# Performance work log

Measured on AMD Instinct MI355X. Metric: run time of the kernel, lower is better.

## Reference

```python
import jax, jax.numpy as jnp
import numpy as np

N, E = 25000, 400000
D_NODE, D_EDGE_IN, D_EH, D_H, D_DUAL = 128, 16, 128, 256, 128


def layer_norm(x, g, b, eps=1e-5):
    mu = jnp.mean(x, axis=-1, keepdims=True)
    var = jnp.mean((x - mu) ** 2, axis=-1, keepdims=True)
    return (x - mu) * jax.lax.rsqrt(var + eps) * g + b


def setup_inputs() -> dict:
    key = jax.random.key(0)
    ks = jax.random.split(key, 20)

    def w(k, shape):
        return (jax.random.normal(k, shape, dtype=jnp.float32) * 0.05)

    inp = {
        "node_embedding": jax.random.normal(ks[0], (N, D_NODE), dtype=jnp.float32),
        "edge_index": jax.random.randint(ks[1], (2, E), 0, N, dtype=jnp.int64),
        "edge_attr": jax.random.normal(ks[2], (E, D_EDGE_IN), dtype=jnp.float32),
        "dual_node_emb": jax.random.normal(ks[3], (E, D_DUAL), dtype=jnp.float32),
        "atom_reactivity_logits": jax.random.normal(ks[4], (N,), dtype=jnp.float32),
        "W_be1": w(ks[5], (D_EDGE_IN, D_EH)), "b_be1": jnp.zeros((D_EH,), jnp.float32),
        "g_be1": jnp.ones((D_EH,), jnp.float32), "bb_be1": jnp.zeros((D_EH,), jnp.float32),
        "W_be2": w(ks[6], (D_EH, D_EH)), "b_be2": jnp.zeros((D_EH,), jnp.float32),
        "g_be2": jnp.ones((D_EH,), jnp.float32), "bb_be2": jnp.zeros((D_EH,), jnp.float32),
        "W_be3": w(ks[7], (D_EH, D_EH)), "b_be3": jnp.zeros((D_EH,), jnp.float32),
        "g_be3": jnp.ones((D_EH,), jnp.float32), "bb_be3": jnp.zeros((D_EH,), jnp.float32),
        # DualGraphBondReactivityPredictor
        "W_d1": w(ks[8], (D_DUAL, D_H)), "b_d1": jnp.zeros((D_H,), jnp.float32),
        "W_d2": w(ks[9], (D_H, D_H)), "b_d2": jnp.zeros((D_H,), jnp.float32),
        "W_do": w(ks[10], (D_H, 1)), "b_do": jnp.zeros((1,), jnp.float32),
        # main head: in = 2*D_NODE + D_EH + 3 = 387
        "W_f1": w(ks[11], (2 * D_NODE + D_EH + 3, D_H)), "b_f1": jnp.zeros((D_H,), jnp.float32),
        "W_f2": w(ks[12], (D_H, D_H)), "b_f2": jnp.zeros((D_H,), jnp.float32),
        "W_bo": w(ks[13], (D_H, 1)), "b_bo": jnp.zeros((1,), jnp.float32),
    }
    return inp


def reference(node_embedding, edge_index, edge_attr, dual_node_emb, atom_reactivity_logits,
              W_be1, b_be1, g_be1, bb_be1, W_be2, b_be2, g_be2, bb_be2,
              W_be3, b_be3, g_be3, bb_be3,
              W_d1, b_d1, W_d2, b_d2, W_do, b_do,
              W_f1, b_f1, W_f2, b_f2, W_bo, b_bo):
    src, dst = edge_index[0], edge_index[1]

    # BondEmbedding (dropout = identity in eval mode)
    e = jax.nn.silu(layer_norm(edge_attr @ W_be1 + b_be1, g_be1, bb_be1))
    e = jax.nn.silu(layer_norm(e @ W_be2 + b_be2, g_be2, bb_be2))
    e = jax.nn.silu(layer_norm(e @ W_be3 + b_be3, g_be3, bb_be3))  # [E, D_EH]

    atom_p = jax.nn.sigmoid(atom_reactivity_logits)  # [N]
    p_src = atom_p[src][:, None]  # [E,1]
    p_dst = atom_p[dst][:, None]

    # dual-graph bond reactivity
    d = jax.nn.silu(dual_node_emb @ W_d1 + b_d1)
    d = jax.nn.silu(d @ W_d2 + b_d2)
    dual_p = jax.nn.sigmoid((d @ W_do + b_do)[:, 0])[:, None]  # [E,1]

    feats = jnp.concatenate(
        [node_embedding[src], node_embedding[dst], e, dual_p, p_src, p_dst], axis=-1
    )  # [E, 2*D_NODE + D_EH + 3]

    x = jax.nn.silu(feats @ W_f1 + b_f1)
    x = jax.nn.silu(x @ W_f2 + b_f2)
    return (x @ W_bo + b_bo)[:, 0]  # [E]
```

## Files before the change

### kernel.cpp

```cpp
#include <hip/hip_runtime.h>
#include <hip/hip_bf16.h>
#include <stdint.h>

typedef __attribute__((ext_vector_type(8))) short bf16x8;
typedef __attribute__((ext_vector_type(4))) float f32x4;
typedef __attribute__((ext_vector_type(4))) float float4v;

__device__ __forceinline__ uint16_t bfc(float x){
    __hip_bfloat16 h = __float2bfloat16(x);
    return __builtin_bit_cast(uint16_t, h);
}
__device__ __forceinline__ uint32_t pk2(float a, float b){
    return (uint32_t)bfc(a) | ((uint32_t)bfc(b) << 16);
}
__device__ __forceinline__ float fsigmoid(float x){ return 1.0f / (1.0f + __expf(-x)); }
__device__ __forceinline__ float fsilu(float x){ return x * fsigmoid(x); }

__device__ __forceinline__ bf16x8 pack8(float4v lo, float4v hi){
    bf16x8 r;
    r[0]=(short)bfc(lo[0]); r[1]=(short)bfc(lo[1]);
    r[2]=(short)bfc(lo[2]); r[3]=(short)bfc(lo[3]);
    r[4]=(short)bfc(hi[0]); r[5]=(short)bfc(hi[1]);
    r[6]=(short)bfc(hi[2]); r[7]=(short)bfc(hi[3]);
    return r;
}

#define SZ_BE1 4096
#define SZ_128 16384
#define SZ_D1  32768
#define SZ_D2  65536
#define SZ_F1  98304
#define OFF_BE1 0
#define OFF_BE2 (OFF_BE1 + SZ_BE1)
#define OFF_BE3 (OFF_BE2 + SZ_128)
#define OFF_D1  (OFF_BE3 + SZ_128)
#define OFF_D2  (OFF_D1 + SZ_D1)
#define OFF_F1  (OFF_D2 + SZ_D2)
#define OFF_F2  (OFF_F1 + SZ_F1)
#define WS_ELEMS (OFF_F2 + SZ_D2)

__device__ __forceinline__ int fragpos(int k, int c, int OUT){
    int kt = k >> 5, ct = c >> 4;
    int fid = kt * (OUT >> 4) + ct;
    int ln = ((k & 31) >> 3) * 16 + (c & 15);
    return fid * 512 + ln * 8 + (k & 7);
}

__global__ void __launch_bounds__(256)
prep_w(const float* __restrict__ Wbe1, const float* __restrict__ Wbe2,
       const float* __restrict__ Wbe3, const float* __restrict__ Wd1,
       const float* __restrict__ Wd2,  const float* __restrict__ Wf1,
       const float* __restrict__ Wf2,  uint16_t* __restrict__ ws){
    int t = blockIdx.x * 256 + threadIdx.x;
    if (t >= WS_ELEMS) return;
    if (t < OFF_BE2) {
        int u = t;            int k = u >> 7, c = u & 127;
        float v = (k < 16) ? Wbe1[k * 128 + c] : 0.0f;
        ws[OFF_BE1 + fragpos(k, c, 128)] = bfc(v);
    } else if (t < OFF_BE3) {
        int u = t - OFF_BE2;  int k = u >> 7, c = u & 127;
        ws[OFF_BE2 + fragpos(k, c, 128)] = bfc(Wbe2[u]);
    } else if (t < OFF_D1) {
        int u = t - OFF_BE3;  int k = u >> 7, c = u & 127;
        ws[OFF_BE3 + fragpos(k, c, 128)] = bfc(Wbe3[u]);
    } else if (t < OFF_D2) {
        int u = t - OFF_D1;   int k = u >> 8, c = u & 255;
        ws[OFF_D1 + fragpos(k, c, 256)] = bfc(Wd1[u]);
    } else if (t < OFF_F1) {
        int u = t - OFF_D2;   int k = u >> 8, c = u & 255;
        ws[OFF_D2 + fragpos(k, c, 256)] = bfc(Wd2[u]);
    } else if (t < OFF_F2) {
        int u = t - OFF_F1;   int k = u >> 8, c = u & 255;
        ws[OFF_F1 + fragpos(k, c, 256)] = bfc(Wf1[u]);
    } else {
        int u = t - OFF_F2;   int k = u >> 8, c = u & 255;
        ws[OFF_F2 + fragpos(k, c, 256)] = bfc(Wf2[u]);
    }
}

__global__ void __launch_bounds__(256)
prep_n(const float* __restrict__ src, uint16_t* __restrict__ dst, int n){
    int t = blockIdx.x * 256 + threadIdx.x;
    if (t < n) dst[t] = bfc(src[t]);
}

typedef const __attribute__((address_space(1))) void gas_void;
typedef __attribute__((address_space(3))) void las_void;
__device__ __forceinline__ void g2l16(const void* g, void* l){
    __builtin_amdgcn_global_load_lds((gas_void*)g, (las_void*)l, 16, 0, 0);
}

#define LDS_TOTAL 135168

__global__ void __launch_bounds__(512) __attribute__((amdgpu_waves_per_eu(2, 2)))
bond_fast_kernel(const int* __restrict__ edge_index,
                 const float* __restrict__ edge_attr, const float* __restrict__ dual_emb,
                 const float* __restrict__ logits,
                 const float* __restrict__ b_be1, const float* __restrict__ g_be1, const float* __restrict__ bb_be1,
                 const float* __restrict__ b_be2, const float* __restrict__ g_be2, const float* __restrict__ bb_be2,
                 const float* __restrict__ b_be3, const float* __restrict__ g_be3, const float* __restrict__ bb_be3,
                 const float* __restrict__ b_d1, const float* __restrict__ b_d2,
                 const float* __restrict__ W_do, const float* __restrict__ b_do,
                 const float* __restrict__ W_f1, const float* __restrict__ b_f1,
                 const float* __restrict__ b_f2,
                 const float* __restrict__ W_bo, const float* __restrict__ b_bo,
                 const uint16_t* __restrict__ ws, float* __restrict__ out, int E)
{
    __shared__ char lds[LDS_TOTAL];
    const int t    = threadIdx.x;
    const int wave = t >> 6;
    const int lane = t & 63;
    const int li   = lane & 15, lg = lane >> 4;
    const int eg   = wave >> 1;
    const int ch   = wave & 1;
    const int e0b  = blockIdx.x * 128;

    char* bufE = lds;
    char* h256 = lds + 32768;
    uint16_t* wb0 = (uint16_t*)(lds + 98304);
    uint16_t* wb1 = (uint16_t*)(lds + 114688);
    float* ps  = (float*)(lds + 131072);
    float* pd  = (float*)(lds + 131584);
    int* sidx  = (int*)(lds + 132096);
    int* didx  = (int*)(lds + 132608);
    float* dpp = (float*)(lds + 133120);
    float* bop = (float*)(lds + 134144);

    const uint8_t*  wsb = (const uint8_t*)ws;
    const uint16_t* nbf = ws + WS_ELEMS;

    if (t < 128) {
        int e = e0b + t; if (e >= E) e = E - 1;
        int s_ = edge_index[e];
        int d_ = edge_index[E + e];
        sidx[t] = s_; didx[t] = d_;
        ps[t] = fsigmoid(logits[s_]);
        pd[t] = fsigmoid(logits[d_]);
    }

    int cur = 0;
    auto stageW = [&](int elemoff, int big){
        uint8_t* dst = (uint8_t*)(cur ? wb0 : wb1) + t * 16;
        const uint8_t* g = wsb + (size_t)elemoff * 2 + t * 16;
        g2l16(g, dst);
        if (big) g2l16(g + 8192, dst + 8192);
    };
    auto stepend = [&](){ __syncthreads(); cur ^= 1; };
    auto curbuf  = [&]() -> const uint16_t* { return cur ? wb1 : wb0; };

    f32x4 acc[2][8];

    auto ldf = [&](const uint16_t* w, int fid) -> bf16x8 {
        return *(const bf16x8*)(w + fid * 512 + lane * 8);
    };
    auto grpBE = [&](const uint16_t* w, bf16x8 a0){
        #pragma unroll
        for (int ct = 0; ct < 8; ++ct){
            bf16x8 b = ldf(w, ct);
            acc[0][ct] = __builtin_amdgcn_mfma_f32_16x16x32_bf16(a0, b, acc[0][ct], 0, 0, 0);
        }
    };
    auto grp256 = [&](const uint16_t* w, bf16x8 a0, bf16x8 a1){
        #pragma unroll
        for (int ct = 0; ct < 8; ++ct){
            bf16x8 b = ldf(w, ch * 8 + ct);
            acc[0][ct] = __builtin_amdgcn_mfma_f32_16x16x32_bf16(a0, b, acc[0][ct], 0, 0, 0);
            acc[1][ct] = __builtin_amdgcn_mfma_f32_16x16x32_bf16(a1, b, acc[1][ct], 0, 0, 0);
        }
    };
    auto initBE = [&](const float* b){
        #pragma unroll
        for (int ct = 0; ct < 8; ++ct){
            float bv = b[li + 16 * ct];
            f32x4 iv = {bv, bv, bv, bv};
            acc[0][ct] = iv;
        }
    };
    auto init256 = [&](const float* b){
        #pragma unroll
        for (int ct = 0; ct < 8; ++ct){
            float bv = b[ch * 128 + ct * 16 + li];
            f32x4 iv = {bv, bv, bv, bv};
            acc[0][ct] = iv; acc[1][ct] = iv;
        }
    };
    auto eb_read = [&](int row, int kt) -> bf16x8 {
        int off = row * 256 + (kt * 32 + lg * 8) * 2;
        return *(const bf16x8*)(bufE + (off ^ ((row & 7) << 4)));
    };
    auto h2_read = [&](int row, int kt) -> bf16x8 {
        int off = row * 512 + (kt * 32 + lg * 8) * 2;
        return *(const bf16x8*)(h256 + (off ^ ((row & 7) << 4)));
    };
    auto lnstoreBE = [&](const float* g, const float* bb){
        #pragma unroll
        for (int r = 0; r < 4; ++r){
            float s = 0.f, q = 0.f;
            #pragma unroll
            for (int ct = 0; ct < 8; ++ct){ float v = acc[0][ct][r]; s += v; q += v*v; }
            s += __shfl_xor(s, 1); q += __shfl_xor(q, 1);
            s += __shfl_xor(s, 2); q += __shfl_xor(q, 2);
            s += __shfl_xor(s, 4); q += __shfl_xor(q, 4);
            s += __shfl_xor(s, 8); q += __shfl_xor(q, 8);
            float mu = s * 0.0078125f;
            float var = q * 0.0078125f - mu * mu;
            float rs = rsqrtf(var + 1e-5f);
            int row = wave * 16 + lg * 4 + r;
            int rswz = (row & 7) << 4;
            #pragma unroll
            for (int ct = 0; ct < 8; ++ct){
                int col = li + 16 * ct;
                float v = (acc[0][ct][r] - mu) * rs * g[col] + bb[col];
                int off = row * 256 + col * 2;
                *(uint16_t*)(bufE + (off ^ rswz)) = bfc(fsilu(v));
            }
        }
    };
    auto silustore256 = [&](){
        #pragma unroll
        for (int rt = 0; rt < 2; ++rt){
            #pragma unroll
            for (int r = 0; r < 4; ++r){
                int row = eg * 32 + rt * 16 + lg * 4 + r;
                int rswz = (row & 7) << 4;
                #pragma unroll
                for (int ct = 0; ct < 8; ++ct){
                    int off = row * 512 + (ch * 128 + ct * 16 + li) * 2;
                    *(uint16_t*)(h256 + (off ^ rswz)) = bfc(fsilu(acc[rt][ct][r]));
                }
            }
        }
    };

    {
        const uint8_t* g = wsb + t * 16;
        g2l16(g, (uint8_t*)wb0 + t * 16);
    }
    __syncthreads();

    {
        stageW(OFF_BE2, 0);
        bf16x8 aE = {0,0,0,0,0,0,0,0};
        if (lg < 2){
            int ea = e0b + wave * 16 + li; if (ea >= E) ea = E - 1;
            const float* pa = edge_attr + (size_t)ea * 16 + lg * 8;
            aE = pack8(*(const float4v*)pa, *(const float4v*)(pa + 4));
        }
        initBE(b_be1);
        grpBE(curbuf(), aE);
        lnstoreBE(g_be1, bb_be1);
        stepend();
    }

    initBE(b_be2);
    #pragma unroll
    for (int kt = 0; kt < 4; ++kt){
        if (kt < 3) stageW(OFF_BE2 + (kt + 1) * 4096, 0);
        else        stageW(OFF_BE3, 0);
        grpBE(curbuf(), eb_read(wave * 16 + li, kt));
        if (kt == 3) lnstoreBE(g_be2, bb_be2);
        stepend();
    }
    initBE(b_be3);
    #pragma unroll
    for (int kt = 0; kt < 4; ++kt){
        if (kt < 3) stageW(OFF_BE3 + (kt + 1) * 4096, 0);
        else        stageW(OFF_D1, 1);
        grpBE(curbuf(), eb_read(wave * 16 + li, kt));
        if (kt == 3) lnstoreBE(g_be3, bb_be3);
        stepend();
    }

    init256(b_d1);
    #pragma unroll
    for (int kt = 0; kt < 4; ++kt){
        float4v va0, va1, vb0, vb1;
        {
            int ea = e0b + eg * 32 + li;      if (ea >= E) ea = E - 1;
            int eb = e0b + eg * 32 + 16 + li; if (eb >= E) eb = E - 1;
            const float* pa = dual_emb + (size_t)ea * 128 + kt * 32 + lg * 8;
            const float* pb = dual_emb + (size_t)eb * 128 + kt * 32 + lg * 8;
            va0 = *(const float4v*)pa; va1 = *(const float4v*)(pa + 4);
            vb0 = *(const float4v*)pb; vb1 = *(const float4v*)(pb + 4);
        }
        if (kt < 3) stageW(OFF_D1 + (kt + 1) * 8192, 1);
        else        stageW(OFF_D2, 1);
        grp256(curbuf(), pack8(va0, va1), pack8(vb0, vb1));
        if (kt == 3) silustore256();
        stepend();
    }

    init256(b_d2);
    #pragma unroll
    for (int kt = 0; kt < 8; ++kt){
        if (kt < 7) stageW(OFF_D2 + (kt + 1) * 8192, 1);
        else        stageW(OFF_F1, 1);
        grp256(curbuf(), h2_read(eg * 32 + li, kt), h2_read(eg * 32 + 16 + li, kt));
        if (kt == 7){
            #pragma unroll
            for (int rt = 0; rt < 2; ++rt){
                #pragma unroll
                for (int r = 0; r < 4; ++r){
                    float s = 0.f;
                    #pragma unroll
                    for (int ct = 0; ct < 8; ++ct)
                        s += fsilu(acc[rt][ct][r]) * W_do[ch * 128 + ct * 16 + li];
                    s += __shfl_xor(s, 1); s += __shfl_xor(s, 2);
                    s += __shfl_xor(s, 4); s += __shfl_xor(s, 8);
                    if (li == 0) dpp[ch * 128 + eg * 32 + rt * 16 + lg * 4 + r] = s;
                }
            }
        }
        stepend();
    }

    {
        {
            float bdo0 = b_do[0];
            #pragma unroll
            for (int ct = 0; ct < 8; ++ct){
                int col = ch * 128 + ct * 16 + li;
                float bv = b_f1[col];
                float t0 = W_f1[384 * 256 + col];
                float t1 = W_f1[385 * 256 + col];
                float t2 = W_f1[386 * 256 + col];
                #pragma unroll
                for (int rt = 0; rt < 2; ++rt)
                    #pragma unroll
                    for (int r = 0; r < 4; ++r){
                        int row = eg * 32 + rt * 16 + lg * 4 + r;
                        float dv = fsigmoid(dpp[row] + dpp[128 + row] + bdo0);
                        acc[rt][ct][r] = bv + dv*t0 + ps[row]*t1 + pd[row]*t2;
                    }
            }
        }
        int s0 = sidx[eg * 32 + li],      s1 = sidx[eg * 32 + 16 + li];
        int d0 = didx[eg * 32 + li],      d1 = didx[eg * 32 + 16 + li];
        #pragma unroll
        for (int kt = 0; kt < 12; ++kt){
            bf16x8 a0, a1;
            if (kt < 8){
                int ra = (kt < 4) ? s0 : d0;
                int rb = (kt < 4) ? s1 : d1;
                int ko = (kt & 3) * 32 + lg * 8;
                a0 = *(const bf16x8*)(nbf + (size_t)ra * 128 + ko);
                a1 = *(const bf16x8*)(nbf + (size_t)rb * 128 + ko);
            } else {
                a0 = eb_read(eg * 32 + li, kt - 8);
                a1 = eb_read(eg * 32 + 16 + li, kt - 8);
            }
            if (kt < 11) stageW(OFF_F1 + (kt + 1) * 8192, 1);
            else         stageW(OFF_F2, 1);
            grp256(curbuf(), a0, a1);
            if (kt == 11) silustore256();
            stepend();
        }
    }

    init256(b_f2);
    #pragma unroll
    for (int kt = 0; kt < 8; ++kt){
        if (kt < 7) stageW(OFF_F2 + (kt + 1) * 8192, 1);
        grp256(curbuf(), h2_read(eg * 32 + li, kt), h2_read(eg * 32 + 16 + li, kt));
        if (kt == 7){
            #pragma unroll
            for (int rt = 0; rt < 2; ++rt){
                #pragma unroll
                for (int r = 0; r < 4; ++r){
                    float s = 0.f;
                    #pragma unroll
                    for (int ct = 0; ct < 8; ++ct)
                        s += fsilu(acc[rt][ct][r]) * W_bo[ch * 128 + ct * 16 + li];
                    s += __shfl_xor(s, 1); s += __shfl_xor(s, 2);
                    s += __shfl_xor(s, 4); s += __shfl_xor(s, 8);
                    if (li == 0) bop[ch * 128 + eg * 32 + rt * 16 + lg * 4 + r] = s;
                }
            }
        } else {
            stepend();
        }
    }
    __syncthreads();
    if (t < 128){
        int e = e0b + t;
        if (e < E) out[e] = bop[t] + bop[128 + t] + b_bo[0];
    }
}

__global__ void __launch_bounds__(512) __attribute__((amdgpu_waves_per_eu(2, 2)))
bond_fused_kernel(const float* __restrict__ node_emb, const int* __restrict__ edge_index,
                  const float* __restrict__ edge_attr, const float* __restrict__ dual_emb,
                  const float* __restrict__ logits,
                  const float* __restrict__ W_be1, const float* __restrict__ b_be1,
                  const float* __restrict__ g_be1, const float* __restrict__ bb_be1,
                  const float* __restrict__ W_be2, const float* __restrict__ b_be2,
                  const float* __restrict__ g_be2, const float* __restrict__ bb_be2,
                  const float* __restrict__ W_be3, const float* __restrict__ b_be3,
                  const float* __restrict__ g_be3, const float* __restrict__ bb_be3,
                  const float* __restrict__ W_d1, const float* __restrict__ b_d1,
                  const float* __restrict__ W_d2, const float* __restrict__ b_d2,
                  const float* __restrict__ W_do, const float* __restrict__ b_do,
                  const float* __restrict__ W_f1, const float* __restrict__ b_f1,
                  const float* __restrict__ W_f2, const float* __restrict__ b_f2,
                  const float* __restrict__ W_bo, const float* __restrict__ b_bo,
                  float* __restrict__ out, int E)
{
    __shared__ char lds[LDS_TOTAL];
    const int t    = threadIdx.x;
    const int wave = t >> 6;
    const int lane = t & 63;
    const int li   = lane & 15, lg = lane >> 4;
    const int eg   = wave >> 1;
    const int ch   = wave & 1;
    const int e0b  = blockIdx.x * 128;

    char* bufE = lds;
    char* h256 = lds + 32768;
    uint16_t* wb0 = (uint16_t*)(lds + 98304);
    uint16_t* wb1 = (uint16_t*)(lds + 114688);
    float* ps  = (float*)(lds + 131072);
    float* pd  = (float*)(lds + 131584);
    int* sidx  = (int*)(lds + 132096);
    int* didx  = (int*)(lds + 132608);
    float* dpp = (float*)(lds + 133120);
    float* bop = (float*)(lds + 134144);

    if (t < 128) {
        int e = e0b + t; if (e >= E) e = E - 1;
        int s_ = edge_index[e];
        int d_ = edge_index[E + e];
        sidx[t] = s_; didx[t] = d_;
        ps[t] = fsigmoid(logits[s_]);
        pd[t] = fsigmoid(logits[d_]);
    }

    float sr[2][8];
    auto issueW256 = [&](const float* W, int kbase){
        #pragma unroll
        for (int h = 0; h < 2; ++h){
            const float* p = W + (size_t)(kbase + lg * 8) * 256 + (wave + 8*h) * 16 + li;
            #pragma unroll
            for (int j = 0; j < 8; ++j) sr[h][j] = p[j * 256];
        }
    };
    auto issueW128 = [&](const float* W, int kbase, int K){
        const float* p = W + (size_t)(kbase + lg * 8) * 128 + wave * 16 + li;
        #pragma unroll
        for (int j = 0; j < 8; ++j)
            sr[0][j] = (kbase + lg * 8 + j < K) ? p[j * 128] : 0.f;
    };
    auto commitW = [&](uint16_t* dst, int nh){
        #pragma unroll
        for (int h = 0; h < 2; ++h){
            if (h < nh){
                uint4 w;
                w.x = pk2(sr[h][0], sr[h][1]); w.y = pk2(sr[h][2], sr[h][3]);
                w.z = pk2(sr[h][4], sr[h][5]); w.w = pk2(sr[h][6], sr[h][7]);
                *(uint4*)(dst + (wave + 8*h) * 512 + lane * 8) = w;
            }
        }
    };

    int cur = 0;
    auto stepend = [&](int mode){
        if (mode) commitW(cur ? wb0 : wb1, mode == 128 ? 1 : 2);
        __syncthreads();
        cur ^= 1;
    };
    auto curbuf = [&]() -> const uint16_t* { return cur ? wb1 : wb0; };

    f32x4 acc[2][8];

    auto ldf = [&](const uint16_t* w, int fid) -> bf16x8 {
        return *(const bf16x8*)(w + fid * 512 + lane * 8);
    };
    auto grpBE = [&](const uint16_t* w, bf16x8 a0){
        #pragma unroll
        for (int ct = 0; ct < 8; ++ct){
            bf16x8 b = ldf(w, ct);
            acc[0][ct] = __builtin_amdgcn_mfma_f32_16x16x32_bf16(a0, b, acc[0][ct], 0, 0, 0);
        }
    };
    auto grp256 = [&](const uint16_t* w, bf16x8 a0, bf16x8 a1){
        #pragma unroll
        for (int ct = 0; ct < 8; ++ct){
            bf16x8 b = ldf(w, ch * 8 + ct);
            acc[0][ct] = __builtin_amdgcn_mfma_f32_16x16x32_bf16(a0, b, acc[0][ct], 0, 0, 0);
            acc[1][ct] = __builtin_amdgcn_mfma_f32_16x16x32_bf16(a1, b, acc[1][ct], 0, 0, 0);
        }
    };
    auto initBE = [&](const float* b){
        #pragma unroll
        for (int ct = 0; ct < 8; ++ct){
            float bv = b[li + 16 * ct];
            f32x4 iv = {bv, bv, bv, bv};
            acc[0][ct] = iv;
        }
    };
    auto init256 = [&](const float* b){
        #pragma unroll
        for (int ct = 0; ct < 8; ++ct){
            float bv = b[ch * 128 + ct * 16 + li];
            f32x4 iv = {bv, bv, bv, bv};
            acc[0][ct] = iv; acc[1][ct] = iv;
        }
    };
    auto eb_read = [&](int row, int kt) -> bf16x8 {
        int off = row * 256 + (kt * 32 + lg * 8) * 2;
        return *(const bf16x8*)(bufE + (off ^ ((row & 7) << 4)));
    };
    auto h2_read = [&](int row, int kt) -> bf16x8 {
        int off = row * 512 + (kt * 32 + lg * 8) * 2;
        return *(const bf16x8*)(h256 + (off ^ ((row & 7) << 4)));
    };
    auto lnstoreBE = [&](const float* g, const float* bb){
        #pragma unroll
        for (int r = 0; r < 4; ++r){
            float s = 0.f, q = 0.f;
            #pragma unroll
            for (int ct = 0; ct < 8; ++ct){ float v = acc[0][ct][r]; s += v; q += v*v; }
            s += __shfl_xor(s, 1); q += __shfl_xor(q, 1);
            s += __shfl_xor(s, 2); q += __shfl_xor(q, 2);
            s += __shfl_xor(s, 4); q += __shfl_xor(q, 4);
            s += __shfl_xor(s, 8); q += __shfl_xor(q, 8);
            float mu = s * 0.0078125f;
            float var = q * 0.0078125f - mu * mu;
            float rs = rsqrtf(var + 1e-5f);
            int row = wave * 16 + lg * 4 + r;
            int rswz = (row & 7) << 4;
            #pragma unroll
            for (int ct = 0; ct < 8; ++ct){
                int col = li + 16 * ct;
                float v = (acc[0][ct][r] - mu) * rs * g[col] + bb[col];
                int off = row * 256 + col * 2;
                *(uint16_t*)(bufE + (off ^ rswz)) = bfc(fsilu(v));
            }
        }
    };
    auto silustore256 = [&](){
        #pragma unroll
        for (int rt = 0; rt < 2; ++rt){
            #pragma unroll
            for (int r = 0; r < 4; ++r){
                int row = eg * 32 + rt * 16 + lg * 4 + r;
                int rswz = (row & 7) << 4;
                #pragma unroll
                for (int ct = 0; ct < 8; ++ct){
                    int off = row * 512 + (ch * 128 + ct * 16 + li) * 2;
                    *(uint16_t*)(h256 + (off ^ rswz)) = bfc(fsilu(acc[rt][ct][r]));
                }
            }
        }
    };

    issueW128(W_be1, 0, 16);
    commitW(wb0, 1);
    __syncthreads();

    {
        bf16x8 aE = {0,0,0,0,0,0,0,0};
        if (lg < 2){
            int ea = e0b + wave * 16 + li; if (ea >= E) ea = E - 1;
            const float* pa = edge_attr + (size_t)ea * 16 + lg * 8;
            aE = pack8(*(const float4v*)pa, *(const float4v*)(pa + 4));
        }
        issueW128(W_be2, 0, 128);
        initBE(b_be1);
        grpBE(curbuf(), aE);
        lnstoreBE(g_be1, bb_be1);
        stepend(128);
    }

    initBE(b_be2);
    #pragma unroll 1
    for (int kt = 0; kt < 4; ++kt){
        if (kt < 3) issueW128(W_be2, (kt + 1) * 32, 128);
        else        issueW128(W_be3, 0, 128);
        grpBE(curbuf(), eb_read(wave * 16 + li, kt));
        if (kt == 3) lnstoreBE(g_be2, bb_be2);
        stepend(128);
    }
    initBE(b_be3);
    #pragma unroll 1
    for (int kt = 0; kt < 4; ++kt){
        if (kt < 3) issueW128(W_be3, (kt + 1) * 32, 128);
        else        issueW256(W_d1, 0);
        grpBE(curbuf(), eb_read(wave * 16 + li, kt));
        if (kt == 3) lnstoreBE(g_be3, bb_be3);
        stepend(kt < 3 ? 128 : 256);
    }

    init256(b_d1);
    #pragma unroll 1
    for (int kt = 0; kt < 4; ++kt){
        float4v va0, va1, vb0, vb1;
        {
            int ea = e0b + eg * 32 + li;      if (ea >= E) ea = E - 1;
            int eb = e0b + eg * 32 + 16 + li; if (eb >= E) eb = E - 1;
            const float* pa = dual_emb + (size_t)ea * 128 + kt * 32 + lg * 8;
            const float* pb = dual_emb + (size_t)eb * 128 + kt * 32 + lg * 8;
            va0 = *(const float4v*)pa; va1 = *(const float4v*)(pa + 4);
            vb0 = *(const float4v*)pb; vb1 = *(const float4v*)(pb + 4);
        }
        if (kt < 3) issueW256(W_d1, (kt + 1) * 32);
        else        issueW256(W_d2, 0);
        grp256(curbuf(), pack8(va0, va1), pack8(vb0, vb1));
        if (kt == 3) silustore256();
        stepend(256);
    }

    init256(b_d2);
    #pragma unroll 1
    for (int kt = 0; kt < 8; ++kt){
        if (kt < 7) issueW256(W_d2, (kt + 1) * 32);
        else        issueW256(W_f1, 0);
        grp256(curbuf(), h2_read(eg * 32 + li, kt), h2_read(eg * 32 + 16 + li, kt));
        if (kt == 7){
            #pragma unroll
            for (int rt = 0; rt < 2; ++rt){
                #pragma unroll
                for (int r = 0; r < 4; ++r){
                    float s = 0.f;
                    #pragma unroll
                    for (int ct = 0; ct < 8; ++ct)
                        s += fsilu(acc[rt][ct][r]) * W_do[ch * 128 + ct * 16 + li];
                    s += __shfl_xor(s, 1); s += __shfl_xor(s, 2);
                    s += __shfl_xor(s, 4); s += __shfl_xor(s, 8);
                    if (li == 0) dpp[ch * 128 + eg * 32 + rt * 16 + lg * 4 + r] = s;
                }
            }
        }
        stepend(256);
    }

    {
        {
            float bdo0 = b_do[0];
            #pragma unroll
            for (int ct = 0; ct < 8; ++ct){
                int col = ch * 128 + ct * 16 + li;
                float bv = b_f1[col];
                float t0 = W_f1[384 * 256 + col];
                float t1 = W_f1[385 * 256 + col];
                float t2 = W_f1[386 * 256 + col];
                #pragma unroll
                for (int rt = 0; rt < 2; ++rt)
                    #pragma unroll
                    for (int r = 0; r < 4; ++r){
                        int row = eg * 32 + rt * 16 + lg * 4 + r;
                        float dv = fsigmoid(dpp[row] + dpp[128 + row] + bdo0);
                        acc[rt][ct][r] = bv + dv*t0 + ps[row]*t1 + pd[row]*t2;
                    }
            }
        }
        int s0 = sidx[eg * 32 + li],      s1 = sidx[eg * 32 + 16 + li];
        int d0 = didx[eg * 32 + li],      d1 = didx[eg * 32 + 16 + li];
        #pragma unroll 1
        for (int kt = 0; kt < 12; ++kt){
            bf16x8 a0, a1;
            if (kt < 8){
                int ra = (kt < 4) ? s0 : d0;
                int rb = (kt < 4) ? s1 : d1;
                int ko = (kt & 3) * 32 + lg * 8;
                const float* pa = node_emb + (size_t)ra * 128 + ko;
                const float* pb = node_emb + (size_t)rb * 128 + ko;
                a0 = pack8(*(const float4v*)pa, *(const float4v*)(pa + 4));
                a1 = pack8(*(const float4v*)pb, *(const float4v*)(pb + 4));
            } else {
                a0 = eb_read(eg * 32 + li, kt - 8);
                a1 = eb_read(eg * 32 + 16 + li, kt - 8);
            }
            if (kt < 11) issueW256(W_f1, (kt + 1) * 32);
            else         issueW256(W_f2, 0);
            grp256(curbuf(), a0, a1);
            if (kt == 11) silustore256();
            stepend(256);
        }
    }

    init256(b_f2);
    #pragma unroll 1
    for (int kt = 0; kt < 8; ++kt){
        if (kt < 7) issueW256(W_f2, (kt + 1) * 32);
        grp256(curbuf(), h2_read(eg * 32 + li, kt), h2_read(eg * 32 + 16 + li, kt));
        if (kt == 7){
            #pragma unroll
            for (int rt = 0; rt < 2; ++rt){
                #pragma unroll
                for (int r = 0; r < 4; ++r){
                    float s = 0.f;
                    #pragma unroll
                    for (int ct = 0; ct < 8; ++ct)
                        s += fsilu(acc[rt][ct][r]) * W_bo[ch * 128 + ct * 16 + li];
                    s += __shfl_xor(s, 1); s += __shfl_xor(s, 2);
                    s += __shfl_xor(s, 4); s += __shfl_xor(s, 8);
                    if (li == 0) bop[ch * 128 + eg * 32 + rt * 16 + lg * 4 + r] = s;
                }
            }
        } else {
            stepend(256);
        }
    }
    __syncthreads();
    if (t < 128){
        int e = e0b + t;
        if (e < E) out[e] = bop[t] + bop[128 + t] + b_bo[0];
    }
}

extern "C" void kernel_launch(void* const* d_in, const int* in_sizes, int n_in,
                              void* d_out, int out_size, void* d_ws, size_t ws_size,
                              hipStream_t stream) {
    const float* node_emb   = (const float*)d_in[0];
    const int*   edge_index = (const int*)d_in[1];
    const float* edge_attr  = (const float*)d_in[2];
    const float* dual_emb   = (const float*)d_in[3];
    const float* logits     = (const float*)d_in[4];
    const float* W_be1 = (const float*)d_in[5];
    const float* b_be1 = (const float*)d_in[6];
    const float* g_be1 = (const float*)d_in[7];
    const float* bb_be1= (const float*)d_in[8];
    const float* W_be2 = (const float*)d_in[9];
    const float* b_be2 = (const float*)d_in[10];
    const float* g_be2 = (const float*)d_in[11];
    const float* bb_be2= (const float*)d_in[12];
    const float* W_be3 = (const float*)d_in[13];
    const float* b_be3 = (const float*)d_in[14];
    const float* g_be3 = (const float*)d_in[15];
    const float* bb_be3= (const float*)d_in[16];
    const float* W_d1  = (const float*)d_in[17];
    const float* b_d1  = (const float*)d_in[18];
    const float* W_d2  = (const float*)d_in[19];
    const float* b_d2  = (const float*)d_in[20];
    const float* W_do  = (const float*)d_in[21];
    const float* b_do  = (const float*)d_in[22];
    const float* W_f1  = (const float*)d_in[23];
    const float* b_f1  = (const float*)d_in[24];
    const float* W_f2  = (const float*)d_in[25];
    const float* b_f2  = (const float*)d_in[26];
    const float* W_bo  = (const float*)d_in[27];
    const float* b_bo  = (const float*)d_in[28];
    float* out = (float*)d_out;

    int E = in_sizes[2] / 16;
    int nblocks = (E + 127) / 128;
    size_t nodeElems = (size_t)in_sizes[0];
    size_t wsNeed = ((size_t)WS_ELEMS + nodeElems) * 2;

    if (ws_size >= wsNeed) {
        uint16_t* ws16 = (uint16_t*)d_ws;
        prep_w<<<dim3((WS_ELEMS + 255) / 256), dim3(256), 0, stream>>>(
            W_be1, W_be2, W_be3, W_d1, W_d2, W_f1, W_f2, ws16);
        prep_n<<<dim3((int)((nodeElems + 255) / 256)), dim3(256), 0, stream>>>(
            node_emb, ws16 + WS_ELEMS, (int)nodeElems);
        bond_fast_kernel<<<dim3(nblocks), dim3(512), 0, stream>>>(
            edge_index, edge_attr, dual_emb, logits,
            b_be1, g_be1, bb_be1,
            b_be2, g_be2, bb_be2,
            b_be3, g_be3, bb_be3,
            b_d1, b_d2, W_do, b_do,
            W_f1, b_f1, b_f2, W_bo, b_bo,
            ws16, out, E);
    } else {
        bond_fused_kernel<<<dim3(nblocks), dim3(512), 0, stream>>>(
            node_emb, edge_index, edge_attr, dual_emb, logits,
            W_be1, b_be1, g_be1, bb_be1,
            W_be2, b_be2, g_be2, bb_be2,
            W_be3, b_be3, g_be3, bb_be3,
            W_d1, b_d1, W_d2, b_d2, W_do, b_do,
            W_f1, b_f1, W_f2, b_f2, W_bo, b_bo,
            out, E);
    }
}
```

Before: 708.3 us.

## Read MFMA weight fragments straight from global, shrink LDS and tile to raise occupancy

The fast kernel stops staging weight fragments into double-buffered LDS with global_load_lds and per-step barriers. Each wave now loads its B fragments directly from the global bf16 weight buffer, relying on L2 for reuse. The block tile drops from 128 to 64 edges, with each wave owning a 32-column slice. Only four waves run the bond-embedding layers, and partial output dot products are reduced across eight waves. LDS use falls to about 54 KB and waves_per_eu rises to 4 to fit more blocks per CU, at the cost of more global and L2 traffic for weights and less reuse of each B fragment.

```diff
diff --git a/kernel.cpp b/kernel.cpp
--- a/kernel.cpp
+++ b/kernel.cpp
@@ -84,15 +84,9 @@
     if (t < n) dst[t] = bfc(src[t]);
 }
 
-typedef const __attribute__((address_space(1))) void gas_void;
-typedef __attribute__((address_space(3))) void las_void;
-__device__ __forceinline__ void g2l16(const void* g, void* l){
-    __builtin_amdgcn_global_load_lds((gas_void*)g, (las_void*)l, 16, 0, 0);
-}
-
-#define LDS_TOTAL 135168
-
-__global__ void __launch_bounds__(512) __attribute__((amdgpu_waves_per_eu(2, 2)))
+#define LDS_FAST 54528
+
+__global__ void __launch_bounds__(512) __attribute__((amdgpu_waves_per_eu(4, 4)))
 bond_fast_kernel(const int* __restrict__ edge_index,
                  const float* __restrict__ edge_attr, const float* __restrict__ dual_emb,
                  const float* __restrict__ logits,
@@ -106,30 +100,27 @@
                  const float* __restrict__ W_bo, const float* __restrict__ b_bo,
                  const uint16_t* __restrict__ ws, float* __restrict__ out, int E)
 {
-    __shared__ char lds[LDS_TOTAL];
+    __shared__ char lds[LDS_FAST];
     const int t    = threadIdx.x;
     const int wave = t >> 6;
     const int lane = t & 63;
     const int li   = lane & 15, lg = lane >> 4;
-    const int eg   = wave >> 1;
-    const int ch   = wave & 1;
-    const int e0b  = blockIdx.x * 128;
+    const int ch   = wave;
+    const int e0b  = blockIdx.x * 64;
 
     char* bufE = lds;
-    char* h256 = lds + 32768;
-    uint16_t* wb0 = (uint16_t*)(lds + 98304);
-    uint16_t* wb1 = (uint16_t*)(lds + 114688);
-    float* ps  = (float*)(lds + 131072);
-    float* pd  = (float*)(lds + 131584);
-    int* sidx  = (int*)(lds + 132096);
-    int* didx  = (int*)(lds + 132608);
-    float* dpp = (float*)(lds + 133120);
-    float* bop = (float*)(lds + 134144);
-
-    const uint8_t*  wsb = (const uint8_t*)ws;
+    char* h256 = lds + 16384;
+    float* ps  = (float*)(lds + 49152);
+    float* pd  = (float*)(lds + 49408);
+    int* sidx  = (int*)(lds + 49664);
+    int* didx  = (int*)(lds + 49920);
+    float* dpp = (float*)(lds + 50176);
+    float* bop = (float*)(lds + 52224);
+    float* dpv = (float*)(lds + 54272);
+
     const uint16_t* nbf = ws + WS_ELEMS;
 
-    if (t < 128) {
+    if (t < 64) {
         int e = e0b + t; if (e >= E) e = E - 1;
         int s_ = edge_index[e];
         int d_ = edge_index[E + e];
@@ -138,66 +129,42 @@
         pd[t] = fsigmoid(logits[d_]);
     }
 
-    int cur = 0;
-    auto stageW = [&](int elemoff, int big){
-        uint8_t* dst = (uint8_t*)(cur ? wb0 : wb1) + t * 16;
-        const uint8_t* g = wsb + (size_t)elemoff * 2 + t * 16;
-        g2l16(g, dst);
-        if (big) g2l16(g + 8192, dst + 8192);
-    };
-    auto stepend = [&](){ __syncthreads(); cur ^= 1; };
-    auto curbuf  = [&]() -> const uint16_t* { return cur ? wb1 : wb0; };
-
-    f32x4 acc[2][8];
-
-    auto ldf = [&](const uint16_t* w, int fid) -> bf16x8 {
-        return *(const bf16x8*)(w + fid * 512 + lane * 8);
-    };
-    auto grpBE = [&](const uint16_t* w, bf16x8 a0){
-        #pragma unroll
-        for (int ct = 0; ct < 8; ++ct){
-            bf16x8 b = ldf(w, ct);
-            acc[0][ct] = __builtin_amdgcn_mfma_f32_16x16x32_bf16(a0, b, acc[0][ct], 0, 0, 0);
-        }
-    };
-    auto grp256 = [&](const uint16_t* w, bf16x8 a0, bf16x8 a1){
-        #pragma unroll
-        for (int ct = 0; ct < 8; ++ct){
-            bf16x8 b = ldf(w, ch * 8 + ct);
-            acc[0][ct] = __builtin_amdgcn_mfma_f32_16x16x32_bf16(a0, b, acc[0][ct], 0, 0, 0);
-            acc[1][ct] = __builtin_amdgcn_mfma_f32_16x16x32_bf16(a1, b, acc[1][ct], 0, 0, 0);
-        }
+    f32x4 acc[8];
+
+    auto ldgB = [&](int elemoff, int fid) -> bf16x8 {
+        return *(const bf16x8*)(ws + elemoff + fid * 512 + lane * 8);
+    };
+    auto eb_read = [&](int row, int kt) -> bf16x8 {
+        int off = row * 256 + (kt * 32 + lg * 8) * 2;
+        return *(const bf16x8*)(bufE + (off ^ ((row & 7) << 4)));
+    };
+    auto h2_read = [&](int row, int kt) -> bf16x8 {
+        int off = row * 512 + (kt * 32 + lg * 8) * 2;
+        return *(const bf16x8*)(h256 + (off ^ ((row & 7) << 4)));
     };
     auto initBE = [&](const float* b){
         #pragma unroll
         for (int ct = 0; ct < 8; ++ct){
             float bv = b[li + 16 * ct];
             f32x4 iv = {bv, bv, bv, bv};
-            acc[0][ct] = iv;
+            acc[ct] = iv;
         }
     };
     auto init256 = [&](const float* b){
         #pragma unroll
-        for (int ct = 0; ct < 8; ++ct){
-            float bv = b[ch * 128 + ct * 16 + li];
+        for (int ct = 0; ct < 2; ++ct){
+            float bv = b[ch * 32 + ct * 16 + li];
             f32x4 iv = {bv, bv, bv, bv};
-            acc[0][ct] = iv; acc[1][ct] = iv;
-        }
-    };
-    auto eb_read = [&](int row, int kt) -> bf16x8 {
-        int off = row * 256 + (kt * 32 + lg * 8) * 2;
-        return *(const bf16x8*)(bufE + (off ^ ((row & 7) << 4)));
-    };
-    auto h2_read = [&](int row, int kt) -> bf16x8 {
-        int off = row * 512 + (kt * 32 + lg * 8) * 2;
-        return *(const bf16x8*)(h256 + (off ^ ((row & 7) << 4)));
+            #pragma unroll
+            for (int rt = 0; rt < 4; ++rt) acc[rt * 2 + ct] = iv;
+        }
     };
     auto lnstoreBE = [&](const float* g, const float* bb){
         #pragma unroll
         for (int r = 0; r < 4; ++r){
             float s = 0.f, q = 0.f;
             #pragma unroll
-            for (int ct = 0; ct < 8; ++ct){ float v = acc[0][ct][r]; s += v; q += v*v; }
+            for (int ct = 0; ct < 8; ++ct){ float v = acc[ct][r]; s += v; q += v*v; }
             s += __shfl_xor(s, 1); q += __shfl_xor(q, 1);
             s += __shfl_xor(s, 2); q += __shfl_xor(q, 2);
             s += __shfl_xor(s, 4); q += __shfl_xor(q, 4);
@@ -210,7 +177,7 @@
             #pragma unroll
             for (int ct = 0; ct < 8; ++ct){
                 int col = li + 16 * ct;
-                float v = (acc[0][ct][r] - mu) * rs * g[col] + bb[col];
+                float v = (acc[ct][r] - mu) * rs * g[col] + bb[col];
                 int off = row * 256 + col * 2;
                 *(uint16_t*)(bufE + (off ^ rswz)) = bfc(fsilu(v));
             }
@@ -218,175 +185,206 @@
     };
     auto silustore256 = [&](){
         #pragma unroll
-        for (int rt = 0; rt < 2; ++rt){
+        for (int rt = 0; rt < 4; ++rt){
             #pragma unroll
             for (int r = 0; r < 4; ++r){
-                int row = eg * 32 + rt * 16 + lg * 4 + r;
+                int row = rt * 16 + lg * 4 + r;
                 int rswz = (row & 7) << 4;
                 #pragma unroll
-                for (int ct = 0; ct < 8; ++ct){
-                    int off = row * 512 + (ch * 128 + ct * 16 + li) * 2;
-                    *(uint16_t*)(h256 + (off ^ rswz)) = bfc(fsilu(acc[rt][ct][r]));
+                for (int ct = 0; ct < 2; ++ct){
+                    int off = row * 512 + (ch * 32 + ct * 16 + li) * 2;
+                    *(uint16_t*)(h256 + (off ^ rswz)) = bfc(fsilu(acc[rt * 2 + ct][r]));
                 }
             }
         }
     };
 
-    {
-        const uint8_t* g = wsb + t * 16;
-        g2l16(g, (uint8_t*)wb0 + t * 16);
-    }
-    __syncthreads();
-
-    {
-        stageW(OFF_BE2, 0);
-        bf16x8 aE = {0,0,0,0,0,0,0,0};
-        if (lg < 2){
-            int ea = e0b + wave * 16 + li; if (ea >= E) ea = E - 1;
-            const float* pa = edge_attr + (size_t)ea * 16 + lg * 8;
-            aE = pack8(*(const float4v*)pa, *(const float4v*)(pa + 4));
-        }
-        initBE(b_be1);
-        grpBE(curbuf(), aE);
-        lnstoreBE(g_be1, bb_be1);
-        stepend();
-    }
-
-    initBE(b_be2);
-    #pragma unroll
-    for (int kt = 0; kt < 4; ++kt){
-        if (kt < 3) stageW(OFF_BE2 + (kt + 1) * 4096, 0);
-        else        stageW(OFF_BE3, 0);
-        grpBE(curbuf(), eb_read(wave * 16 + li, kt));
-        if (kt == 3) lnstoreBE(g_be2, bb_be2);
-        stepend();
-    }
-    initBE(b_be3);
-    #pragma unroll
-    for (int kt = 0; kt < 4; ++kt){
-        if (kt < 3) stageW(OFF_BE3 + (kt + 1) * 4096, 0);
-        else        stageW(OFF_D1, 1);
-        grpBE(curbuf(), eb_read(wave * 16 + li, kt));
-        if (kt == 3) lnstoreBE(g_be3, bb_be3);
-        stepend();
+    if (wave < 4){
+        const int erow = wave * 16 + li;
+        {
+            initBE(b_be1);
+            bf16x8 aE = {0,0,0,0,0,0,0,0};
+            if (lg < 2){
+                int ea = e0b + wave * 16 + li; if (ea >= E) ea = E - 1;
+                const float* pa = edge_attr + (size_t)ea * 16 + lg * 8;
+                aE = pack8(*(const float4v*)pa, *(const float4v*)(pa + 4));
+            }
+            #pragma unroll
+            for (int ct = 0; ct < 8; ++ct)
+                acc[ct] = __builtin_amdgcn_mfma_f32_16x16x32_bf16(aE, ldgB(OFF_BE1, ct), acc[ct], 0, 0, 0);
+            lnstoreBE(g_be1, bb_be1);
+        }
+        {
+            initBE(b_be2);
+            #pragma unroll
+            for (int kt = 0; kt < 4; ++kt){
+                bf16x8 a = eb_read(erow, kt);
+                #pragma unroll
+                for (int ct = 0; ct < 8; ++ct)
+                    acc[ct] = __builtin_amdgcn_mfma_f32_16x16x32_bf16(a, ldgB(OFF_BE2, kt * 8 + ct), acc[ct], 0, 0, 0);
+            }
+            lnstoreBE(g_be2, bb_be2);
+        }
+        {
+            initBE(b_be3);
+            #pragma unroll
+            for (int kt = 0; kt < 4; ++kt){
+                bf16x8 a = eb_read(erow, kt);
+                #pragma unroll
+                for (int ct = 0; ct < 8; ++ct)
+                    acc[ct] = __builtin_amdgcn_mfma_f32_16x16x32_bf16(a, ldgB(OFF_BE3, kt * 8 + ct), acc[ct], 0, 0, 0);
+            }
+            lnstoreBE(g_be3, bb_be3);
+        }
     }
 
     init256(b_d1);
     #pragma unroll
     for (int kt = 0; kt < 4; ++kt){
-        float4v va0, va1, vb0, vb1;
-        {
-            int ea = e0b + eg * 32 + li;      if (ea >= E) ea = E - 1;
-            int eb = e0b + eg * 32 + 16 + li; if (eb >= E) eb = E - 1;
+        bf16x8 a[4];
+        #pragma unroll
+        for (int rt = 0; rt < 4; ++rt){
+            int ea = e0b + rt * 16 + li; if (ea >= E) ea = E - 1;
             const float* pa = dual_emb + (size_t)ea * 128 + kt * 32 + lg * 8;
-            const float* pb = dual_emb + (size_t)eb * 128 + kt * 32 + lg * 8;
-            va0 = *(const float4v*)pa; va1 = *(const float4v*)(pa + 4);
-            vb0 = *(const float4v*)pb; vb1 = *(const float4v*)(pb + 4);
-        }
-        if (kt < 3) stageW(OFF_D1 + (kt + 1) * 8192, 1);
-        else        stageW(OFF_D2, 1);
-        grp256(curbuf(), pack8(va0, va1), pack8(vb0, vb1));
-        if (kt == 3) silustore256();
-        stepend();
-    }
+            a[rt] = pack8(*(const float4v*)pa, *(const float4v*)(pa + 4));
+        }
+        bf16x8 b0 = ldgB(OFF_D1, kt * 16 + ch * 2);
+        bf16x8 b1 = ldgB(OFF_D1, kt * 16 + ch * 2 + 1);
+        #pragma unroll
+        for (int rt = 0; rt < 4; ++rt){
+            acc[rt*2]   = __builtin_amdgcn_mfma_f32_16x16x32_bf16(a[rt], b0, acc[rt*2],   0, 0, 0);
+            acc[rt*2+1] = __builtin_amdgcn_mfma_f32_16x16x32_bf16(a[rt], b1, acc[rt*2+1], 0, 0, 0);
+        }
+    }
+    silustore256();
+    __syncthreads();
 
     init256(b_d2);
     #pragma unroll
     for (int kt = 0; kt < 8; ++kt){
-        if (kt < 7) stageW(OFF_D2 + (kt + 1) * 8192, 1);
-        else        stageW(OFF_F1, 1);
-        grp256(curbuf(), h2_read(eg * 32 + li, kt), h2_read(eg * 32 + 16 + li, kt));
-        if (kt == 7){
-            #pragma unroll
-            for (int rt = 0; rt < 2; ++rt){
-                #pragma unroll
-                for (int r = 0; r < 4; ++r){
-                    float s = 0.f;
-                    #pragma unroll
-                    for (int ct = 0; ct < 8; ++ct)
-                        s += fsilu(acc[rt][ct][r]) * W_do[ch * 128 + ct * 16 + li];
-                    s += __shfl_xor(s, 1); s += __shfl_xor(s, 2);
-                    s += __shfl_xor(s, 4); s += __shfl_xor(s, 8);
-                    if (li == 0) dpp[ch * 128 + eg * 32 + rt * 16 + lg * 4 + r] = s;
-                }
-            }
-        }
-        stepend();
-    }
-
+        bf16x8 a[4];
+        #pragma unroll
+        for (int rt = 0; rt < 4; ++rt) a[rt] = h2_read(rt * 16 + li, kt);
+        bf16x8 b0 = ldgB(OFF_D2, kt * 16 + ch * 2);
+        bf16x8 b1 = ldgB(OFF_D2, kt * 16 + ch * 2 + 1);
+        #pragma unroll
+        for (int rt = 0; rt < 4; ++rt){
+            acc[rt*2]   = __builtin_amdgcn_mfma_f32_16x16x32_bf16(a[rt], b0, acc[rt*2],   0, 0, 0);
+            acc[rt*2+1] = __builtin_amdgcn_mfma_f32_16x16x32_bf16(a[rt], b1, acc[rt*2+1], 0, 0, 0);
+        }
+    }
     {
-        {
-            float bdo0 = b_do[0];
-            #pragma unroll
-            for (int ct = 0; ct < 8; ++ct){
-                int col = ch * 128 + ct * 16 + li;
+        float w0 = W_do[ch * 32 + li], w1 = W_do[ch * 32 + 16 + li];
+        #pragma unroll
+        for (int rt = 0; rt < 4; ++rt){
+            #pragma unroll
+            for (int r = 0; r < 4; ++r){
+                float s = fsilu(acc[rt*2][r]) * w0 + fsilu(acc[rt*2+1][r]) * w1;
+                s += __shfl_xor(s, 1); s += __shfl_xor(s, 2);
+                s += __shfl_xor(s, 4); s += __shfl_xor(s, 8);
+                if (li == 0) dpp[ch * 64 + rt * 16 + lg * 4 + r] = s;
+            }
+        }
+    }
+    __syncthreads();
+    if (t < 64){
+        float s = b_do[0];
+        #pragma unroll
+        for (int i = 0; i < 8; ++i) s += dpp[i * 64 + t];
+        dpv[t] = fsigmoid(s);
+    }
+    __syncthreads();
+
+    {
+        int sv[4], dvi[4];
+        #pragma unroll
+        for (int rt = 0; rt < 4; ++rt){ sv[rt] = sidx[rt*16+li]; dvi[rt] = didx[rt*16+li]; }
+        #pragma unroll
+        for (int rt = 0; rt < 4; ++rt){
+            float dvv[4], psr[4], pdr[4];
+            #pragma unroll
+            for (int r = 0; r < 4; ++r){
+                int row = rt * 16 + lg * 4 + r;
+                dvv[r] = dpv[row]; psr[r] = ps[row]; pdr[r] = pd[row];
+            }
+            #pragma unroll
+            for (int ct = 0; ct < 2; ++ct){
+                int col = ch * 32 + ct * 16 + li;
                 float bv = b_f1[col];
                 float t0 = W_f1[384 * 256 + col];
                 float t1 = W_f1[385 * 256 + col];
                 float t2 = W_f1[386 * 256 + col];
                 #pragma unroll
-                for (int rt = 0; rt < 2; ++rt)
-                    #pragma unroll
-                    for (int r = 0; r < 4; ++r){
-                        int row = eg * 32 + rt * 16 + lg * 4 + r;
-                        float dv = fsigmoid(dpp[row] + dpp[128 + row] + bdo0);
-                        acc[rt][ct][r] = bv + dv*t0 + ps[row]*t1 + pd[row]*t2;
-                    }
-            }
-        }
-        int s0 = sidx[eg * 32 + li],      s1 = sidx[eg * 32 + 16 + li];
-        int d0 = didx[eg * 32 + li],      d1 = didx[eg * 32 + 16 + li];
+                for (int r = 0; r < 4; ++r)
+                    acc[rt*2+ct][r] = bv + dvv[r]*t0 + psr[r]*t1 + pdr[r]*t2;
+            }
+        }
         #pragma unroll
         for (int kt = 0; kt < 12; ++kt){
-            bf16x8 a0, a1;
+            bf16x8 a[4];
             if (kt < 8){
-                int ra = (kt < 4) ? s0 : d0;
-                int rb = (kt < 4) ? s1 : d1;
                 int ko = (kt & 3) * 32 + lg * 8;
-                a0 = *(const bf16x8*)(nbf + (size_t)ra * 128 + ko);
-                a1 = *(const bf16x8*)(nbf + (size_t)rb * 128 + ko);
+                #pragma unroll
+                for (int rt = 0; rt < 4; ++rt){
+                    int row = (kt < 4) ? sv[rt] : dvi[rt];
+                    a[rt] = *(const bf16x8*)(nbf + (size_t)row * 128 + ko);
+                }
             } else {
-                a0 = eb_read(eg * 32 + li, kt - 8);
-                a1 = eb_read(eg * 32 + 16 + li, kt - 8);
-            }
-            if (kt < 11) stageW(OFF_F1 + (kt + 1) * 8192, 1);
-            else         stageW(OFF_F2, 1);
-            grp256(curbuf(), a0, a1);
-            if (kt == 11) silustore256();
-            stepend();
-        }
-    }
+                #pragma unroll
+                for (int rt = 0; rt < 4; ++rt) a[rt] = eb_read(rt * 16 + li, kt - 8);
+            }
+            bf16x8 b0 = ldgB(OFF_F1, kt * 16 + ch * 2);
+            bf16x8 b1 = ldgB(OFF_F1, kt * 16 + ch * 2 + 1);
+            #pragma unroll
+            for (int rt = 0; rt < 4; ++rt){
+                acc[rt*2]   = __builtin_amdgcn_mfma_f32_16x16x32_bf16(a[rt], b0, acc[rt*2],   0, 0, 0);
+                acc[rt*2+1] = __builtin_amdgcn_mfma_f32_16x16x32_bf16(a[rt], b1, acc[rt*2+1], 0, 0, 0);
+            }
+        }
+        silustore256();
+    }
+    __syncthreads();
 
     init256(b_f2);
     #pragma unroll
     for (int kt = 0; kt < 8; ++kt){
-        if (kt < 7) stageW(OFF_F2 + (kt + 1) * 8192, 1);
-        grp256(curbuf(), h2_read(eg * 32 + li, kt), h2_read(eg * 32 + 16 + li, kt));
-        if (kt == 7){
-            #pragma unroll
-            for (int rt = 0; rt < 2; ++rt){
-                #pragma unroll
-                for (int r = 0; r < 4; ++r){
-                    float s = 0.f;
-                    #pragma unroll
-                    for (int ct = 0; ct < 8; ++ct)
-                        s += fsilu(acc[rt][ct][r]) * W_bo[ch * 128 + ct * 16 + li];
-                    s += __shfl_xor(s, 1); s += __shfl_xor(s, 2);
-                    s += __shfl_xor(s, 4); s += __shfl_xor(s, 8);
-                    if (li == 0) bop[ch * 128 + eg * 32 + rt * 16 + lg * 4 + r] = s;
-                }
-            }
-        } else {
-            stepend();
+        bf16x8 a[4];
+        #pragma unroll
+        for (int rt = 0; rt < 4; ++rt) a[rt] = h2_read(rt * 16 + li, kt);
+        bf16x8 b0 = ldgB(OFF_F2, kt * 16 + ch * 2);
+        bf16x8 b1 = ldgB(OFF_F2, kt * 16 + ch * 2 + 1);
+        #pragma unroll
+        for (int rt = 0; rt < 4; ++rt){
+            acc[rt*2]   = __builtin_amdgcn_mfma_f32_16x16x32_bf16(a[rt], b0, acc[rt*2],   0, 0, 0);
+            acc[rt*2+1] = __builtin_amdgcn_mfma_f32_16x16x32_bf16(a[rt], b1, acc[rt*2+1], 0, 0, 0);
+        }
+    }
+    {
+        float w0 = W_bo[ch * 32 + li], w1 = W_bo[ch * 32 + 16 + li];
+        #pragma unroll
+        for (int rt = 0; rt < 4; ++rt){
+            #pragma unroll
+            for (int r = 0; r < 4; ++r){
+                float s = fsilu(acc[rt*2][r]) * w0 + fsilu(acc[rt*2+1][r]) * w1;
+                s += __shfl_xor(s, 1); s += __shfl_xor(s, 2);
+                s += __shfl_xor(s, 4); s += __shfl_xor(s, 8);
+                if (li == 0) bop[ch * 64 + rt * 16 + lg * 4 + r] = s;
+            }
         }
     }
     __syncthreads();
-    if (t < 128){
+    if (t < 64){
         int e = e0b + t;
-        if (e < E) out[e] = bop[t] + bop[128 + t] + b_bo[0];
-    }
-}
-
+        if (e < E){
+            float s = b_bo[0];
+            #pragma unroll
+            for (int i = 0; i < 8; ++i) s += bop[i * 64 + t];
+            out[e] = s;
+        }
+    }
+}
+
+#define LDS_TOTAL_FB 135168
 __global__ void __launch_bounds__(512) __attribute__((amdgpu_waves_per_eu(2, 2)))
 bond_fused_kernel(const float* __restrict__ node_emb, const int* __restrict__ edge_index,
                   const float* __restrict__ edge_attr, const float* __restrict__ dual_emb,
@@ -405,7 +403,7 @@
                   const float* __restrict__ W_bo, const float* __restrict__ b_bo,
                   float* __restrict__ out, int E)
 {
-    __shared__ char lds[LDS_TOTAL];
+    __shared__ char lds[LDS_TOTAL_FB];
     const int t    = threadIdx.x;
     const int wave = t >> 6;
     const int lane = t & 63;
@@ -743,7 +741,6 @@
     float* out = (float*)d_out;
 
     int E = in_sizes[2] / 16;
-    int nblocks = (E + 127) / 128;
     size_t nodeElems = (size_t)in_sizes[0];
     size_t wsNeed = ((size_t)WS_ELEMS + nodeElems) * 2;
 
@@ -753,6 +750,7 @@
             W_be1, W_be2, W_be3, W_d1, W_d2, W_f1, W_f2, ws16);
         prep_n<<<dim3((int)((nodeElems + 255) / 256)), dim3(256), 0, stream>>>(
             node_emb, ws16 + WS_ELEMS, (int)nodeElems);
+        int nblocks = (E + 63) / 64;
         bond_fast_kernel<<<dim3(nblocks), dim3(512), 0, stream>>>(
             edge_index, edge_attr, dual_emb, logits,
             b_be1, g_be1, bb_be1,
@@ -762,6 +760,7 @@
             W_f1, b_f1, b_f2, W_bo, b_bo,
             ws16, out, E);
     } else {
+        int nblocks = (E + 127) / 128;
         bond_fused_kernel<<<dim3(nblocks), dim3(512), 0, stream>>>(
             node_emb, edge_index, edge_attr, dual_emb, logits,
             W_be1, b_be1, g_be1, bb_be1,
```

Measured after the change: 1.011 ms. 42.7% more time.
